# Kernel optimization log

Hardware: AMD Instinct MI355X
Metric: run time of the kernel (lower is better)

Reference implementation:

```python
import jax, jax.numpy as jnp
import numpy as np

SCALE = 2
K_UP = 5
PAD_UNF = (K_UP // 2) * SCALE  # nn.Unfold padding = k_up//2 * scale = 4
BN_INV = float(1.0 / np.sqrt(1.0 + 1e-5))  # BN inference with running_mean=0, running_var=1


def conv2d(x, w, pad):
    return jax.lax.conv_general_dilated(
        x, w, window_strides=(1, 1), padding=[(pad, pad), (pad, pad)],
        dimension_numbers=('NCHW', 'OIHW', 'NCHW'))


def bn(x, g, b):
    return x * (g * BN_INV)[None, :, None, None] + b[None, :, None, None]


def upsample_bilinear_ac(x, oh, ow):
    # bilinear, align_corners=True
    b, c, h, w = x.shape
    ys = jnp.linspace(0.0, h - 1.0, oh)
    xs = jnp.linspace(0.0, w - 1.0, ow)
    y0 = jnp.floor(ys).astype(jnp.int32)
    x0 = jnp.floor(xs).astype(jnp.int32)
    y1 = jnp.minimum(y0 + 1, h - 1)
    x1 = jnp.minimum(x0 + 1, w - 1)
    wy = (ys - y0)[:, None]  # (oh,1)
    wx = (xs - x0)          # (ow,)
    top = x[:, :, y0, :]
    bot = x[:, :, y1, :]
    top = top[:, :, :, x0] * (1.0 - wx) + top[:, :, :, x1] * wx
    bot = bot[:, :, :, x0] * (1.0 - wx) + bot[:, :, :, x1] * wx
    return top * (1.0 - wy) + bot * wy


def setup_inputs() -> dict:
    key = jax.random.key(0)
    ks = jax.random.split(key, 16)
    B, N, C = 4, 4096, 128  # h=w=64
    CL, CM, OUT = 128, 64, 128
    R = C // 4

    def rn(k, shape, s=0.05):
        return s * jax.random.normal(k, shape, dtype=jnp.float32)

    d = {}
    d['x_h'] = rn(ks[0], (B, N, C), 1.0)
    d['x_l'] = rn(ks[1], (B, N * SCALE * SCALE, CL), 1.0)
    # conv_reduce 3x3 C->C
    d['wr'] = rn(ks[2], (C, C, 3, 3))
    d['wr_g'] = jnp.ones((C,), jnp.float32); d['wr_b'] = jnp.zeros((C,), jnp.float32)
    # conv1 1x1 C->CM
    d['w1'] = rn(ks[3], (CM, C, 1, 1))
    d['w1_g'] = jnp.ones((CM,), jnp.float32); d['w1_b'] = jnp.zeros((CM,), jnp.float32)
    # conv2 1x1 2*CL->CM
    d['w2'] = rn(ks[4], (CM, 2 * CL, 1, 1))
    d['w2_g'] = jnp.ones((CM,), jnp.float32); d['w2_b'] = jnp.zeros((CM,), jnp.float32)
    # enc 3x3 2*CM -> k_up^2
    d['we'] = rn(ks[5], (K_UP * K_UP, 2 * CM, 3, 3))
    d['we_g'] = jnp.ones((K_UP * K_UP,), jnp.float32); d['we_b'] = jnp.zeros((K_UP * K_UP,), jnp.float32)
    # channel attention fc1/fc2 (1x1 convs with bias)
    d['wf1'] = rn(ks[6], (R, C, 1, 1)); d['bf1'] = jnp.zeros((R,), jnp.float32)
    d['wf2'] = rn(ks[7], (C, R, 1, 1)); d['bf2'] = jnp.zeros((C,), jnp.float32)
    # conv_out: 3x3 (C+CL)->OUT, then 1x1 OUT->OUT
    d['wo1'] = rn(ks[8], (OUT, C + CL, 3, 3))
    d['wo1_g'] = jnp.ones((OUT,), jnp.float32); d['wo1_b'] = jnp.zeros((OUT,), jnp.float32)
    d['wo2'] = rn(ks[9], (OUT, OUT, 1, 1))
    d['wo2_g'] = jnp.ones((OUT,), jnp.float32); d['wo2_b'] = jnp.zeros((OUT,), jnp.float32)
    return d


def reference(x_h, x_l, wr, wr_g, wr_b, w1, w1_g, w1_b, w2, w2_g, w2_b,
              we, we_g, we_b, wf1, bf1, wf2, bf2,
              wo1, wo1_g, wo1_b, wo2, wo2_g, wo2_b):
    B, N, C = x_h.shape
    h = int(round(N ** 0.5)); w = h
    h_, w_ = h * SCALE, w * SCALE
    xh = jnp.transpose(x_h, (0, 2, 1)).reshape(B, C, h, w)
    xl = jnp.transpose(x_l, (0, 2, 1)).reshape(B, -1, h_, w_)

    # x1 = upsample(conv1(x_h))
    x1 = upsample_bilinear_ac(jax.nn.relu(bn(conv2d(xh, w1, 0), w1_g, w1_b)), h_, w_)

    # channel attention on x_l
    g_c = jnp.mean(xl, axis=(2, 3), keepdims=True)  # (B,CL,1,1)
    g_c = conv2d(g_c, wf1, 0) + bf1[None, :, None, None]
    g_c = jax.nn.relu(g_c)
    g_c = conv2d(g_c, wf2, 0) + bf2[None, :, None, None]
    g_c = jax.nn.sigmoid(g_c) * xl

    x2 = jax.nn.relu(bn(conv2d(jnp.concatenate((g_c, xl), axis=1), w2, 0), w2_g, w2_b))

    # kernel prediction + softmax over k_up^2
    Wk = bn(conv2d(jnp.concatenate((x1, x2), axis=1), we, 1), we_g, we_b)
    Wk = jax.nn.softmax(Wk, axis=1)  # (B, 25, h_, w_)

    # reduce + upsample high-res feature
    xr = jax.nn.relu(bn(conv2d(xh, wr, 1), wr_g, wr_b))
    xup = upsample_bilinear_ac(xr, h_, w_)  # (B, C, h_, w_)

    # CARAFE-style reassembly: accumulate over k_up^2 dilated offsets
    xp = jnp.pad(xup, ((0, 0), (0, 0), (PAD_UNF, PAD_UNF), (PAD_UNF, PAD_UNF)))
    X = jnp.zeros_like(xup)
    idx = 0
    for i in range(K_UP):
        for j in range(K_UP):
            patch = xp[:, :, i * SCALE:i * SCALE + h_, j * SCALE:j * SCALE + w_]
            X = X + patch * Wk[:, idx][:, None]
            idx += 1

    y = jnp.concatenate((X, xl), axis=1)
    y = jax.nn.relu(bn(conv2d(y, wo1, 1), wo1_g, wo1_b))
    y = jax.nn.relu(bn(conv2d(y, wo2, 0), wo2_g, wo2_b))
    return y
```

## Files before the change

### kernel.cpp

```cpp
#include <hip/hip_runtime.h>
#include <hip/hip_bf16.h>

#define BN_INV 0.99999500003749968f

typedef __attribute__((ext_vector_type(8))) short bf16x8;
typedef __attribute__((ext_vector_type(4))) float f32x4;
typedef __attribute__((ext_vector_type(8))) unsigned short ushort8;
typedef unsigned short u16;

__device__ inline u16 f2bf(float f) {
  union { float f; unsigned int u; } v;
  v.f = f;
  unsigned int r = v.u + 0x7FFFu + ((v.u >> 16) & 1u);
  return (u16)(r >> 16);
}
__device__ inline float bf2f(u16 u) {
  union { unsigned int u; float f; } v;
  v.u = ((unsigned int)u) << 16;
  return v.f;
}
__device__ inline float asf(unsigned int u) {
  union { unsigned int u; float f; } v; v.u = u; return v.f;
}
__device__ inline void unpack8(bf16x8 v, float* f) {
  union { bf16x8 v; unsigned int w[4]; } u; u.v = v;
#pragma unroll
  for (int q = 0; q < 4; ++q) {
    f[2 * q]     = asf(u.w[q] << 16);
    f[2 * q + 1] = asf(u.w[q] & 0xFFFF0000u);
  }
}

#define GLOAD_LDS16(g, l)                                              \
  __builtin_amdgcn_global_load_lds(                                    \
      (const __attribute__((address_space(1))) unsigned int*)(g),      \
      (__attribute__((address_space(3))) unsigned int*)(l), 16, 0, 0)

__global__ __launch_bounds__(256) void k_zero_ring_all(
    u16* __restrict__ pad, u16* __restrict__ xcat, u16* __restrict__ xhp) {
  int blk = blockIdx.x;
  u16* buf; int PADW, CH, nb, b0;
  if (blk < 32)      { buf = pad;  PADW = 130; CH = 256; nb = 32; b0 = 0; }
  else if (blk < 48) { buf = xcat; PADW = 130; CH = 128; nb = 16; b0 = 32; }
  else               { buf = xhp;  PADW = 66;  CH = 128; nb = 8;  b0 = 48; }
  int nring = 2 * PADW + 2 * (PADW - 2);
  int vecs = CH >> 3;
  int total = 4 * nring * vecs;
  ushort8 z = {0, 0, 0, 0, 0, 0, 0, 0};
  for (int i = (blk - b0) * 256 + threadIdx.x; i < total; i += nb * 256) {
    int v = i % vecs;
    int r = (i / vecs) % nring;
    int b = i / (vecs * nring);
    int y, x;
    if (r < PADW) { y = 0; x = r; }
    else if (r < 2 * PADW) { y = PADW - 1; x = r - PADW; }
    else { int s = r - 2 * PADW; y = 1 + (s >> 1); x = (s & 1) ? (PADW - 1) : 0; }
    *(ushort8*)(buf + ((size_t)(b * PADW + y) * PADW + x) * CH + v * 8) = z;
  }
}

__global__ __launch_bounds__(256) void k_repack_all(
    const float* __restrict__ wr, const float* __restrict__ wrg,
    const float* __restrict__ we, const float* __restrict__ weg,
    const float* __restrict__ wo1, const float* __restrict__ wo1g,
    const float* __restrict__ wo2, const float* __restrict__ wo2g,
    const float* __restrict__ w1, const float* __restrict__ w1g,
    u16* __restrict__ wr_bf, u16* __restrict__ we_bf, u16* __restrict__ wo1bf,
    u16* __restrict__ wo2bf, u16* __restrict__ w1bf) {
  int blk = blockIdx.x;
  const float *w, *g; u16* out; int Cout, Cin, OPAD, TAPS, base;
  if (blk < 576)       { w = wr;  g = wrg;  out = wr_bf; Cout = 128; Cin = 128; OPAD = 128; TAPS = 9; base = 0; }
  else if (blk < 720)  { w = we;  g = weg;  out = we_bf; Cout = 25;  Cin = 128; OPAD = 32;  TAPS = 9; base = 576; }
  else if (blk < 1872) { w = wo1; g = wo1g; out = wo1bf; Cout = 128; Cin = 256; OPAD = 128; TAPS = 9; base = 720; }
  else if (blk < 1936) { w = wo2; g = wo2g; out = wo2bf; Cout = 128; Cin = 128; OPAD = 128; TAPS = 1; base = 1872; }
  else                 { w = w1;  g = w1g;  out = w1bf;  Cout = 64;  Cin = 128; OPAD = 64;  TAPS = 1; base = 1936; }
  int idx = (blk - base) * 256 + threadIdx.x;
  int c = idx % Cin;
  int o = (idx / Cin) % OPAD;
  int tap = idx / (Cin * OPAD);
  float v = 0.f;
  if (o < Cout) v = w[(o * Cin + c) * TAPS + tap] * g[o] * BN_INV;
  out[idx] = f2bf(v);
}

template <int PADW, int CIN, int NOUT, int NB, int TILE_M, int EPI, int NTHR,
          int WAVES_N>
__global__ __launch_bounds__(NTHR, 1) void k_conv_mfma(
    const u16* __restrict__ pad, const u16* __restrict__ wb,
    const float* __restrict__ bias, void* __restrict__ outp) {
  constexpr int H = PADW - 2;
  constexpr int NSEG = NOUT / NB;
  constexpr int KQ = CIN / 64;
  constexpr int NSTEPS = 9 * KQ;
  constexpr int NWAVES = NTHR / 64;
  constexpr int WAVES_M = NWAVES / WAVES_N;
  constexpr int WN = NB / WAVES_N;
  constexpr int NF = WN / 16;
  constexpr int WM = TILE_M / WAVES_M;
  constexpr int MF = WM / 16;
  constexpr int GRID = 4 * H * NSEG;
  constexpr int CPX = GRID / 8;
  constexpr int ALOADS = TILE_M * 8;
  constexpr int BLOADS = NB * 8;
  __shared__ alignas(16) u16 As[2][TILE_M * 64];
  __shared__ alignas(16) u16 Bs[2][NB * 64];

  int tid = threadIdx.x, wv = tid >> 6, l = tid & 63;
  int wrw = wv / WAVES_N, wc = wv % WAVES_N;
  int bid0 = blockIdx.x;
  int bid = (bid0 & 7) * CPX + (bid0 >> 3);
  int ns = (NSEG > 1) ? (bid % NSEG) : 0;
  int row = (NSEG > 1) ? (bid / NSEG) : bid;
  int b = row / H, y = row % H;
  const u16* pbat = pad + (size_t)b * PADW * PADW * CIN;

  auto stage = [&](int t, int bufi) {
    int tap = t / KQ;
    int ch0 = (t % KQ) * 64;
    int ky = tap / 3, kx = tap % 3;
    const u16* arow = pbat + ((size_t)(y + ky) * PADW + kx) * CIN + ch0;
#pragma unroll
    for (int j = 0; j < ALOADS / NTHR; ++j) {
      int q = j * NTHR + tid;
      int px = q >> 3;
      int sl = (q & 7) ^ (px & 7);
      GLOAD_LDS16(arow + (size_t)px * CIN + sl * 8,
                  (char*)&As[bufi][0] + (size_t)(j * NTHR + (tid & ~63)) * 16);
    }
    const u16* brow = wb + ((size_t)tap * NOUT + ns * NB) * CIN + ch0;
#pragma unroll
    for (int j = 0; j < BLOADS / NTHR; ++j) {
      int q = j * NTHR + tid;
      int co = q >> 3;
      int sl = (q & 7) ^ (co & 7);
      GLOAD_LDS16(brow + (size_t)co * CIN + sl * 8,
                  (char*)&Bs[bufi][0] + (size_t)(j * NTHR + (tid & ~63)) * 16);
    }
    if constexpr (BLOADS % NTHR) {
      if (tid < BLOADS % NTHR) {
        int q = (BLOADS / NTHR) * NTHR + tid;
        int co = q >> 3;
        int sl = (q & 7) ^ (co & 7);
        GLOAD_LDS16(brow + (size_t)co * CIN + sl * 8,
                    (char*)&Bs[bufi][0] +
                        (size_t)((BLOADS / NTHR) * NTHR + (tid & ~63)) * 16);
      }
    }
  };

  f32x4 acc[MF][NF];
#pragma unroll
  for (int m = 0; m < MF; ++m)
#pragma unroll
    for (int n = 0; n < NF; ++n) acc[m][n] = (f32x4){0.f, 0.f, 0.f, 0.f};

  stage(0, 0);
  for (int t = 0; t < NSTEPS; ++t) {
    __syncthreads();
    if (t + 1 < NSTEPS) stage(t + 1, (t + 1) & 1);
    const u16* Ab = &As[t & 1][0];
    const u16* Bb = &Bs[t & 1][0];
    bf16x8 Bf[2][NF];
#pragma unroll
    for (int kf = 0; kf < 2; ++kf)
#pragma unroll
      for (int n = 0; n < NF; ++n) {
        int co = wc * WN + n * 16 + (l & 15);
        int sl = (kf * 4 + (l >> 4)) ^ (co & 7);
        Bf[kf][n] = *(const bf16x8*)((const char*)Bb + co * 128 + sl * 16);
      }
#pragma unroll
    for (int m = 0; m < MF; ++m) {
      int px = wrw * WM + m * 16 + (l & 15);
      int s0 = (l >> 4) ^ (px & 7);
      int s1 = (4 + (l >> 4)) ^ (px & 7);
      bf16x8 a0 = *(const bf16x8*)((const char*)Ab + px * 128 + s0 * 16);
      bf16x8 a1 = *(const bf16x8*)((const char*)Ab + px * 128 + s1 * 16);
#pragma unroll
      for (int n = 0; n < NF; ++n) {
        acc[m][n] = __builtin_amdgcn_mfma_f32_16x16x32_bf16(a0, Bf[0][n], acc[m][n], 0, 0, 0);
        acc[m][n] = __builtin_amdgcn_mfma_f32_16x16x32_bf16(a1, Bf[1][n], acc[m][n], 0, 0, 0);
      }
    }
  }

  int ncol = l & 15, rq = l >> 4;
  size_t pixb = ((size_t)b * H + y) * H;
  if constexpr (EPI == 0) {
    u16* ob = (u16*)outp;
#pragma unroll
    for (int m = 0; m < MF; ++m) {
      int px0 = wrw * WM + m * 16 + rq * 4;
#pragma unroll
      for (int n = 0; n < NF; ++n) {
        int o = ns * NB + wc * WN + n * 16 + ncol;
        float be = bias[o];
#pragma unroll
        for (int r = 0; r < 4; ++r)
          ob[(pixb + px0 + r) * NOUT + o] = f2bf(fmaxf(acc[m][n][r] + be, 0.f));
      }
    }
  } else {
    float* sm = (float*)&As[0][0];
    __syncthreads();
#pragma unroll
    for (int m = 0; m < MF; ++m) {
      int px0 = wrw * WM + m * 16 + rq * 4;
#pragma unroll
      for (int n = 0; n < NF; ++n) {
        int o = wc * WN + n * 16 + ncol;
        float be = (o < 25) ? bias[o] : 0.f;
#pragma unroll
        for (int r = 0; r < 4; ++r)
          sm[(px0 + r) * 33 + o] = acc[m][n][r] + be;
      }
    }
    __syncthreads();
    if (tid < TILE_M) {
      int px = tid;
      float v[25];
      float mx = -1e30f;
#pragma unroll
      for (int i = 0; i < 25; ++i) {
        v[i] = sm[px * 33 + i];
        mx = fmaxf(mx, v[i]);
      }
      float s = 0.f;
#pragma unroll
      for (int i = 0; i < 25; ++i) {
        v[i] = expf(v[i] - mx);
        s += v[i];
      }
      float inv = 1.f / s;
      float* wkp = (float*)outp + (pixb + px) * 25;
#pragma unroll
      for (int i = 0; i < 25; ++i) wkp[i] = v[i] * inv;
    }
  }
}

__global__ __launch_bounds__(256) void k_stage_in(
    const float* __restrict__ xh, const float* __restrict__ xl,
    u16* __restrict__ xhp, u16* __restrict__ pad, float* __restrict__ gpart) {
  int blk = blockIdx.x;
  int tid = threadIdx.x;
  if (blk < 1024) {
    int idx = blk * 256 + tid;
    int c0 = (idx & 15) * 8;
    int p = idx >> 4;
    int b = p >> 12, pp = p & 4095;
    int y = pp >> 6, x = pp & 63;
    const float* s = xh + (size_t)p * 128 + c0;
    ushort8 o;
#pragma unroll
    for (int j = 0; j < 8; ++j) o[j] = f2bf(s[j]);
    *(ushort8*)(xhp + ((size_t)(b * 66 + y + 1) * 66 + (x + 1)) * 128 + c0) = o;
    return;
  }
  int blk2 = blk - 1024;
  int c0 = (tid & 15) * 8;
  int pxl = tid >> 4;
  int b = (blk2 * 64) >> 14;
  float facc[8] = {0.f, 0.f, 0.f, 0.f, 0.f, 0.f, 0.f, 0.f};
#pragma unroll
  for (int it = 0; it < 4; ++it) {
    int p = blk2 * 64 + it * 16 + pxl;
    int pp = p & 16383;
    int y = pp >> 7, x = pp & 127;
    const float* s = xl + (size_t)p * 128 + c0;
    ushort8 o;
#pragma unroll
    for (int j = 0; j < 8; ++j) {
      float f = s[j];
      facc[j] += f;
      o[j] = f2bf(f);
    }
    *(ushort8*)(pad + ((size_t)(b * 130 + y + 1) * 130 + (x + 1)) * 256 + 128 + c0) = o;
  }
  __shared__ float red[16][16][9];
#pragma unroll
  for (int j = 0; j < 8; ++j) red[pxl][tid & 15][j] = facc[j];
  __syncthreads();
  if (tid < 128) {
    float sum = 0.f;
#pragma unroll
    for (int q = 0; q < 16; ++q) sum += red[q][tid >> 3][tid & 7];
    atomicAdd(&gpart[(size_t)(blk2 & 63) * 512 + b * 128 + tid], sum);
  }
}

__global__ __launch_bounds__(128) void k_semlp(
    const float* __restrict__ gpart, const float* __restrict__ wf1,
    const float* __restrict__ bf1, const float* __restrict__ wf2,
    const float* __restrict__ bf2, const float* __restrict__ w2,
    const float* __restrict__ w2g, u16* __restrict__ weffb) {
  int b = blockIdx.x;
  int t = threadIdx.x;
  __shared__ float m[128], hid[32], sg[128];
  float s0 = 0.f;
  for (int s = 0; s < 64; ++s) s0 += gpart[(size_t)s * 512 + b * 128 + t];
  m[t] = s0 * (1.0f / 16384.0f);
  __syncthreads();
  if (t < 32) {
    float a = 0.f;
    for (int c = 0; c < 128; ++c) a += wf1[t * 128 + c] * m[c];
    hid[t] = fmaxf(a + bf1[t], 0.f);
  }
  __syncthreads();
  {
    float a = 0.f;
    for (int r = 0; r < 32; ++r) a += wf2[t * 32 + r] * hid[r];
    a += bf2[t];
    sg[t] = 1.f / (1.f + expf(-a));
  }
  __syncthreads();
  for (int o = 0; o < 64; ++o) {
    float sc = w2g[o] * BN_INV;
    weffb[((size_t)b * 64 + o) * 128 + t] =
        f2bf((w2[o * 256 + t] * sg[t] + w2[o * 256 + 128 + t]) * sc);
  }
}

__global__ __launch_bounds__(256) void k_t1x2(
    const u16* __restrict__ xhp, const u16* __restrict__ w1b,
    const float* __restrict__ w1bias, float* __restrict__ t1,
    const u16* __restrict__ pad, const u16* __restrict__ weffb,
    const float* __restrict__ x2bias, u16* __restrict__ xcat_pad) {
  int t = threadIdx.x;
  int wv = t >> 6, l = t & 63;
  int kg = l >> 4;
  if (blockIdx.x < 256) {
    int blk = blockIdx.x;
    int b = blk >> 6, y = blk & 63;
    int m0 = wv * 16;
    int xc = m0 + (l & 15);
    const u16* abase = xhp + ((size_t)(b * 66 + y + 1) * 66 + xc + 1) * 128 + kg * 8;
    const u16* bbase = w1b + (size_t)(l & 15) * 128 + kg * 8;
    f32x4 acc[4];
#pragma unroll
    for (int i = 0; i < 4; ++i) acc[i] = (f32x4){0.f, 0.f, 0.f, 0.f};
#pragma unroll
    for (int cc = 0; cc < 4; ++cc) {
      bf16x8 a = *(const bf16x8*)(abase + cc * 32);
#pragma unroll
      for (int nf = 0; nf < 4; ++nf) {
        bf16x8 bfr = *(const bf16x8*)(bbase + nf * 16 * 128 + cc * 32);
        acc[nf] = __builtin_amdgcn_mfma_f32_16x16x32_bf16(a, bfr, acc[nf], 0, 0, 0);
      }
    }
    int prow = m0 + (l >> 4) * 4;
    int ncol = l & 15;
    size_t pixb = ((size_t)b << 12) + ((size_t)y << 6);
#pragma unroll
    for (int nf = 0; nf < 4; ++nf) {
      int o = nf * 16 + ncol;
      float be = w1bias[o];
#pragma unroll
      for (int r = 0; r < 4; ++r)
        t1[(pixb + prow + r) * 64 + o] = fmaxf(acc[nf][r] + be, 0.f);
    }
    return;
  }
  int blk = blockIdx.x - 256;
  int b = blk >> 8, rr = blk & 255;
  int y = rr >> 1;
  int xseg = (rr & 1) << 6;
  int m0 = xseg + wv * 16;
  int xc = m0 + (l & 15);
  const u16* abase =
      pad + ((size_t)(b * 130 + y + 1) * 130 + xc + 1) * 256 + 128 + kg * 8;
  const u16* bbase = weffb + (size_t)b * 64 * 128 + (size_t)(l & 15) * 128 + kg * 8;
  f32x4 acc[4];
#pragma unroll
  for (int i = 0; i < 4; ++i) acc[i] = (f32x4){0.f, 0.f, 0.f, 0.f};
#pragma unroll
  for (int cc = 0; cc < 4; ++cc) {
    bf16x8 a = *(const bf16x8*)(abase + cc * 32);
#pragma unroll
    for (int nf = 0; nf < 4; ++nf) {
      bf16x8 bfr = *(const bf16x8*)(bbase + nf * 16 * 128 + cc * 32);
      acc[nf] = __builtin_amdgcn_mfma_f32_16x16x32_bf16(a, bfr, acc[nf], 0, 0, 0);
    }
  }
  int prow = m0 + (l >> 4) * 4;
  int ncol = l & 15;
  size_t rb = (size_t)(b * 130 + y + 1) * 130;
#pragma unroll
  for (int nf = 0; nf < 4; ++nf) {
    int o = nf * 16 + ncol;
    float be = x2bias[o];
#pragma unroll
    for (int r = 0; r < 4; ++r)
      xcat_pad[(rb + prow + r + 1) * 128 + 64 + o] =
          f2bf(fmaxf(acc[nf][r] + be, 0.f));
  }
}

__global__ __launch_bounds__(256) void k_up64_pad(const float* __restrict__ in,
                                                  u16* __restrict__ pad) {
  int t = threadIdx.x;
  int cp = (t & 31) * 2;
  int sub = t >> 5;
  int g = blockIdx.x * 8 + sub;
  int b = g >> 14, pp = g & 16383;
  int oy = pp >> 7, ox = pp & 127;
  const float S = 63.0f / 127.0f;
  float fy = oy * S, fx = ox * S;
  int y0 = (int)fy, x0 = (int)fx;
  int y1 = min(y0 + 1, 63), x1 = min(x0 + 1, 63);
  float wy = fy - y0, wx = fx - x0;
  const float* base = in + (size_t)b * 4096 * 64;
  float2 v00 = *(const float2*)(base + ((y0 << 6) + x0) * 64 + cp);
  float2 v01 = *(const float2*)(base + ((y0 << 6) + x1) * 64 + cp);
  float2 v10 = *(const float2*)(base + ((y1 << 6) + x0) * 64 + cp);
  float2 v11 = *(const float2*)(base + ((y1 << 6) + x1) * 64 + cp);
  float r0 = (v00.x * (1.f - wx) + v01.x * wx) * (1.f - wy) +
             (v10.x * (1.f - wx) + v11.x * wx) * wy;
  float r1 = (v00.y * (1.f - wx) + v01.y * wx) * (1.f - wy) +
             (v10.y * (1.f - wx) + v11.y * wx) * wy;
  ushort2 o2; o2.x = f2bf(r0); o2.y = f2bf(r1);
  *(ushort2*)(pad + ((size_t)(b * 130 + oy + 1) * 130 + ox + 1) * 128 + cp) = o2;
}

__global__ __launch_bounds__(256) void k_up128_bf(
    const u16* __restrict__ in, u16* __restrict__ outb) {
  int t = threadIdx.x;
  int c0 = (t & 15) * 8;
  int px = t >> 4;
  int g = blockIdx.x * 16 + px;
  int b = g >> 14, pp = g & 16383;
  int oy = pp >> 7, ox = pp & 127;
  const float S = 63.0f / 127.0f;
  float fy = oy * S, fx = ox * S;
  int y0 = (int)fy, x0 = (int)fx;
  int y1 = min(y0 + 1, 63), x1 = min(x0 + 1, 63);
  float wy = fy - y0, wx = fx - x0;
  const u16* base = in + (size_t)b * 4096 * 128 + c0;
  bf16x8 v00 = *(const bf16x8*)(base + ((y0 << 6) + x0) * 128);
  bf16x8 v01 = *(const bf16x8*)(base + ((y0 << 6) + x1) * 128);
  bf16x8 v10 = *(const bf16x8*)(base + ((y1 << 6) + x0) * 128);
  bf16x8 v11 = *(const bf16x8*)(base + ((y1 << 6) + x1) * 128);
  float f00[8], f01[8], f10[8], f11[8];
  unpack8(v00, f00); unpack8(v01, f01); unpack8(v10, f10); unpack8(v11, f11);
  ushort8 o;
#pragma unroll
  for (int j = 0; j < 8; ++j) {
    float top = f00[j] * (1.f - wx) + f01[j] * wx;
    float bot = f10[j] * (1.f - wx) + f11[j] * wx;
    o[j] = f2bf(top * (1.f - wy) + bot * wy);
  }
  *(ushort8*)(outb + (size_t)g * 128 + c0) = o;
}

__global__ __launch_bounds__(256) void k_carafe_bf(
    const u16* __restrict__ xup, const float* __restrict__ wk,
    u16* __restrict__ pad) {
  int t = threadIdx.x;
  int c0 = (t & 15) * 8;
  int px = t >> 4;
  int blk = (blockIdx.x & 7) * 512 + (blockIdx.x >> 3);
  int g = blk * 16 + px;
  int b = g >> 14, pp = g & 16383;
  int y = pp >> 7, x = pp & 127;
  __shared__ float wl[16][26];
  for (int i = t; i < 400; i += 256)
    wl[i / 25][i % 25] = wk[(size_t)(blk * 16 + i / 25) * 25 + (i % 25)];
  __syncthreads();
  float acc[8] = {0.f, 0.f, 0.f, 0.f, 0.f, 0.f, 0.f, 0.f};
  const u16* base = xup + ((size_t)b << 14) * 128 + c0;
#pragma unroll
  for (int i = 0; i < 5; ++i) {
    int row = y + 2 * i - 4;
    if ((unsigned)row >= 128u) continue;
#pragma unroll
    for (int jj = 0; jj < 5; ++jj) {
      int col = x + 2 * jj - 4;
      if ((unsigned)col >= 128u) continue;
      bf16x8 v = *(const bf16x8*)(base + (size_t)((row << 7) + col) * 128);
      float w = wl[px][i * 5 + jj];
      float f[8];
      unpack8(v, f);
#pragma unroll
      for (int k = 0; k < 8; ++k) acc[k] += w * f[k];
    }
  }
  ushort8 o;
#pragma unroll
  for (int k = 0; k < 8; ++k) o[k] = f2bf(acc[k]);
  *(ushort8*)(pad + ((size_t)(b * 130 + y + 1) * 130 + (x + 1)) * 256 + c0) = o;
}

__global__ __launch_bounds__(256) void k_wo2_mfma(
    const u16* __restrict__ y1, const u16* __restrict__ wb,
    const float* __restrict__ bb, float* __restrict__ out) {
  int t = threadIdx.x;
  int wv = t >> 6, l = t & 63;
  int blk = blockIdx.x;
  int b = blk >> 8, rr = blk & 255;
  int y = rr >> 1;
  int xseg = (rr & 1) << 6;
  int m0 = xseg + wv * 16;
  int xc = m0 + (l & 15);
  int kg = l >> 4;
  const u16* abase =
      y1 + ((size_t)((b << 14) + (y << 7) + xc)) * 128 + kg * 8;
  const u16* bbase = wb + (size_t)(l & 15) * 128 + kg * 8;
  f32x4 acc[8];
#pragma unroll
  for (int i = 0; i < 8; ++i) acc[i] = (f32x4){0.f, 0.f, 0.f, 0.f};
#pragma unroll
  for (int cc = 0; cc < 4; ++cc) {
    bf16x8 a = *(const bf16x8*)(abase + cc * 32);
#pragma unroll
    for (int nf = 0; nf < 8; ++nf) {
      bf16x8 bfr = *(const bf16x8*)(bbase + nf * 16 * 128 + cc * 32);
      acc[nf] = __builtin_amdgcn_mfma_f32_16x16x32_bf16(a, bfr, acc[nf], 0, 0, 0);
    }
  }
  __shared__ float lds[128 * 65];
  int lpx0 = wv * 16 + (l >> 4) * 4;
  int ncol = l & 15;
#pragma unroll
  for (int nf = 0; nf < 8; ++nf) {
    int o = nf * 16 + ncol;
    float be = bb[o];
#pragma unroll
    for (int r = 0; r < 4; ++r)
      lds[o * 65 + lpx0 + r] = fmaxf(acc[nf][r] + be, 0.f);
  }
  __syncthreads();
  size_t obase = (((size_t)(b * 128)) * 128 + y) * 128 + xseg;
#pragma unroll
  for (int rep = 0; rep < 8; ++rep) {
    int idx = rep * 256 + t;
    int o = idx >> 4;
    int x4 = (idx & 15) * 4;
    f32x4 v;
#pragma unroll
    for (int k = 0; k < 4; ++k) v[k] = lds[o * 65 + x4 + k];
    *(f32x4*)(out + obase + (size_t)o * 16384 + x4) = v;
  }
}

extern "C" void kernel_launch(void* const* d_in, const int* in_sizes, int n_in,
                              void* d_out, int out_size, void* d_ws,
                              size_t ws_size, hipStream_t stream) {
  const float* x_h  = (const float*)d_in[0];
  const float* x_l  = (const float*)d_in[1];
  const float* wr   = (const float*)d_in[2];
  const float* wr_g = (const float*)d_in[3];
  const float* wr_b = (const float*)d_in[4];
  const float* w1   = (const float*)d_in[5];
  const float* w1_g = (const float*)d_in[6];
  const float* w1_b = (const float*)d_in[7];
  const float* w2   = (const float*)d_in[8];
  const float* w2_g = (const float*)d_in[9];
  const float* w2_b = (const float*)d_in[10];
  const float* we   = (const float*)d_in[11];
  const float* we_g = (const float*)d_in[12];
  const float* we_b = (const float*)d_in[13];
  const float* wf1  = (const float*)d_in[14];
  const float* bf1  = (const float*)d_in[15];
  const float* wf2  = (const float*)d_in[16];
  const float* bf2  = (const float*)d_in[17];
  const float* wo1  = (const float*)d_in[18];
  const float* wo1_g= (const float*)d_in[19];
  const float* wo1_b= (const float*)d_in[20];
  const float* wo2  = (const float*)d_in[21];
  const float* wo2_g= (const float*)d_in[22];
  const float* wo2_b= (const float*)d_in[23];
  float* out = (float*)d_out;

  float* ws = (float*)d_ws;
  u16* pad      = (u16*)ws;
  u16* xcat_pad = (u16*)(ws + 8652800);
  u16* xup      = xcat_pad;
  float* wkb   = ws + 12979200;
  float* t1    = ws + 14617600;
  u16* xr = (u16*)t1;
  float* y1reg = ws + 15666176;
  u16* y1     = (u16*)y1reg;
  u16* xh_pad = (u16*)y1reg;
  float* gpart = ws + 19860480;
  u16* weff_bf = (u16*)(gpart + 32768);
  float* tail  = gpart + 32768 + 16384;
  u16* wr_bf = (u16*)tail;
  u16* we_bf = (u16*)(tail + 73728);
  u16* wo1bf = (u16*)(tail + 73728 + 18432);
  u16* wo2bf = (u16*)(tail + 73728 + 18432 + 147456);
  u16* w1bf  = (u16*)(tail + 73728 + 18432 + 147456 + 8192);

  hipMemsetAsync(gpart, 0, 32768 * sizeof(float), stream);
  k_zero_ring_all<<<56, 256, 0, stream>>>(pad, xcat_pad, xh_pad);
  k_repack_all<<<1968, 256, 0, stream>>>(wr, wr_g, we, we_g, wo1, wo1_g,
                                         wo2, wo2_g, w1, w1_g,
                                         wr_bf, we_bf, wo1bf, wo2bf, w1bf);

  k_stage_in<<<2048, 256, 0, stream>>>(x_h, x_l, xh_pad, pad, gpart);
  k_semlp<<<4, 128, 0, stream>>>(gpart, wf1, bf1, wf2, bf2, w2, w2_g, weff_bf);
  k_t1x2<<<1280, 256, 0, stream>>>(xh_pad, w1bf, w1_b, t1,
                                   pad, weff_bf, w2_b, xcat_pad);
  k_up64_pad<<<8192, 256, 0, stream>>>(t1, xcat_pad);

  k_conv_mfma<130, 128, 32, 32, 128, 2, 512, 2><<<512, 512, 0, stream>>>(
      xcat_pad, we_bf, we_b, wkb);
  k_conv_mfma<66, 128, 128, 64, 64, 0, 512, 4><<<512, 512, 0, stream>>>(
      xh_pad, wr_bf, wr_b, xr);
  k_up128_bf<<<4096, 256, 0, stream>>>(xr, xup);
  k_carafe_bf<<<4096, 256, 0, stream>>>(xup, wkb, pad);
  k_conv_mfma<130, 256, 128, 128, 128, 0, 512, 4><<<512, 512, 0, stream>>>(
      pad, wo1bf, wo1_b, y1);
  k_wo2_mfma<<<1024, 256, 0, stream>>>(y1, wo2bf, wo2_b, out);
}
```

Measured before the change: 190.2 us.

## Add dedicated wo1 conv kernel with row-halo LDS staging and prepacked MFMA weight fragments

Replaces the generic MFMA conv for the 256-to-128 channel 3x3 output conv with a specialized kernel. Each block computes one output row, stages three padded input rows per 64-channel chunk into swizzled LDS, and reuses them across all 9 taps. Weights are prepacked into per-lane MFMA fragment order so B operands load straight from global memory without LDS. This is meant to cut redundant input staging and weight shuffling, at the cost of keeping weight loads in global/L2 traffic and having no double buffering between chunks.

```diff
diff --git a/kernel.cpp b/kernel.cpp
--- a/kernel.cpp
+++ b/kernel.cpp
@@ -62,18 +62,16 @@
 __global__ __launch_bounds__(256) void k_repack_all(
     const float* __restrict__ wr, const float* __restrict__ wrg,
     const float* __restrict__ we, const float* __restrict__ weg,
-    const float* __restrict__ wo1, const float* __restrict__ wo1g,
     const float* __restrict__ wo2, const float* __restrict__ wo2g,
     const float* __restrict__ w1, const float* __restrict__ w1g,
-    u16* __restrict__ wr_bf, u16* __restrict__ we_bf, u16* __restrict__ wo1bf,
+    u16* __restrict__ wr_bf, u16* __restrict__ we_bf,
     u16* __restrict__ wo2bf, u16* __restrict__ w1bf) {
   int blk = blockIdx.x;
   const float *w, *g; u16* out; int Cout, Cin, OPAD, TAPS, base;
-  if (blk < 576)       { w = wr;  g = wrg;  out = wr_bf; Cout = 128; Cin = 128; OPAD = 128; TAPS = 9; base = 0; }
-  else if (blk < 720)  { w = we;  g = weg;  out = we_bf; Cout = 25;  Cin = 128; OPAD = 32;  TAPS = 9; base = 576; }
-  else if (blk < 1872) { w = wo1; g = wo1g; out = wo1bf; Cout = 128; Cin = 256; OPAD = 128; TAPS = 9; base = 720; }
-  else if (blk < 1936) { w = wo2; g = wo2g; out = wo2bf; Cout = 128; Cin = 128; OPAD = 128; TAPS = 1; base = 1872; }
-  else                 { w = w1;  g = w1g;  out = w1bf;  Cout = 64;  Cin = 128; OPAD = 64;  TAPS = 1; base = 1936; }
+  if (blk < 576)      { w = wr;  g = wrg;  out = wr_bf; Cout = 128; Cin = 128; OPAD = 128; TAPS = 9; base = 0; }
+  else if (blk < 720) { w = we;  g = weg;  out = we_bf; Cout = 25;  Cin = 128; OPAD = 32;  TAPS = 9; base = 576; }
+  else if (blk < 784) { w = wo2; g = wo2g; out = wo2bf; Cout = 128; Cin = 128; OPAD = 128; TAPS = 1; base = 720; }
+  else                { w = w1;  g = w1g;  out = w1bf;  Cout = 64;  Cin = 128; OPAD = 64;  TAPS = 1; base = 784; }
   int idx = (blk - base) * 256 + threadIdx.x;
   int c = idx % Cin;
   int o = (idx / Cin) % OPAD;
@@ -81,6 +79,21 @@
   float v = 0.f;
   if (o < Cout) v = w[(o * Cin + c) * TAPS + tap] * g[o] * BN_INV;
   out[idx] = f2bf(v);
+}
+
+__global__ __launch_bounds__(256) void k_repack_wo1frag(
+    const float* __restrict__ w, const float* __restrict__ g,
+    u16* __restrict__ out) {
+  int idx = blockIdx.x * 256 + threadIdx.x;
+  int e   = idx & 7;
+  int l   = (idx >> 3) & 63;
+  int kf  = (idx >> 9) & 1;
+  int nf  = (idx >> 10) & 7;
+  int cq  = (idx >> 13) & 3;
+  int tap = idx >> 15;
+  int o = nf * 16 + (l & 15);
+  int c = cq * 64 + (kf * 4 + (l >> 4)) * 8 + e;
+  out[idx] = f2bf(w[(o * 256 + c) * 9 + tap] * g[o] * BN_INV);
 }
 
 template <int PADW, int CIN, int NOUT, int NB, int TILE_M, int EPI, int NTHR,
@@ -235,6 +248,94 @@
       float* wkp = (float*)outp + (pixb + px) * 25;
 #pragma unroll
       for (int i = 0; i < 25; ++i) wkp[i] = v[i] * inv;
+    }
+  }
+}
+
+__global__ __launch_bounds__(512, 1) void k_wo1_conv(
+    const u16* __restrict__ pad, const u16* __restrict__ bfrag,
+    const float* __restrict__ bias, u16* __restrict__ y1) {
+  __shared__ alignas(16) u16 As[3 * 1056 * 8];
+  int tid = threadIdx.x, wv = tid >> 6, l = tid & 63;
+  int wrw = wv >> 2, wc = wv & 3;
+  int bid0 = blockIdx.x;
+  int bid = (bid0 & 7) * 64 + (bid0 >> 3);
+  int b = bid >> 7, y = bid & 127;
+  const u16* pbat = pad + (size_t)b * 130 * 130 * 256;
+
+  f32x4 acc[4][2];
+#pragma unroll
+  for (int m = 0; m < 4; ++m)
+#pragma unroll
+    for (int n = 0; n < 2; ++n) acc[m][n] = (f32x4){0.f, 0.f, 0.f, 0.f};
+
+  for (int cq = 0; cq < 4; ++cq) {
+    __syncthreads();
+    {
+      const u16* base = pbat + (size_t)y * 130 * 256 + cq * 64;
+#pragma unroll
+      for (int j = 0; j < 6; ++j) {
+        int q = j * 512 + tid;
+        int r = q / 1056;
+        int s = q - r * 1056;
+        int px = s >> 3;
+        int sl = (s & 7) ^ (px & 7);
+        GLOAD_LDS16(base + ((size_t)r * 130 + px) * 256 + sl * 8,
+                    (char*)As + (size_t)(j * 512 + (tid & ~63)) * 16);
+      }
+      if (tid < 96) {
+        int q = 3072 + tid;
+        int r = q / 1056;
+        int s = q - r * 1056;
+        int px = s >> 3;
+        int sl = (s & 7) ^ (px & 7);
+        GLOAD_LDS16(base + ((size_t)r * 130 + px) * 256 + sl * 8,
+                    (char*)As + (size_t)(3072 + (tid & ~63)) * 16);
+      }
+    }
+    __syncthreads();
+
+#pragma unroll
+    for (int tap = 0; tap < 9; ++tap) {
+      int ky = tap / 3, kx = tap % 3;
+      bf16x8 Bf[2][2];
+#pragma unroll
+      for (int kf = 0; kf < 2; ++kf)
+#pragma unroll
+        for (int n = 0; n < 2; ++n) {
+          int nf = wc * 2 + n;
+          Bf[kf][n] = *(const bf16x8*)(bfrag +
+              (((((size_t)tap * 4 + cq) * 8 + nf) * 2 + kf) * 64 + l) * 8);
+        }
+      const u16* arow = As + (size_t)ky * 1056 * 8;
+#pragma unroll
+      for (int m = 0; m < 4; ++m) {
+        int px = wrw * 64 + m * 16 + (l & 15) + kx;
+        int s0 = (l >> 4) ^ (px & 7);
+        int s1 = (4 + (l >> 4)) ^ (px & 7);
+        bf16x8 a0 = *(const bf16x8*)(arow + ((size_t)px * 8 + s0) * 8);
+        bf16x8 a1 = *(const bf16x8*)(arow + ((size_t)px * 8 + s1) * 8);
+#pragma unroll
+        for (int n = 0; n < 2; ++n) {
+          acc[m][n] = __builtin_amdgcn_mfma_f32_16x16x32_bf16(a0, Bf[0][n], acc[m][n], 0, 0, 0);
+          acc[m][n] = __builtin_amdgcn_mfma_f32_16x16x32_bf16(a1, Bf[1][n], acc[m][n], 0, 0, 0);
+        }
+      }
+    }
+  }
+
+  int ncol = l & 15, rq2 = l >> 4;
+  size_t pixb = ((size_t)b * 128 + y) * 128;
+#pragma unroll
+  for (int m = 0; m < 4; ++m) {
+    int px0 = wrw * 64 + m * 16 + rq2 * 4;
+#pragma unroll
+    for (int n = 0; n < 2; ++n) {
+      int o = wc * 32 + n * 16 + ncol;
+      float be = bias[o];
+#pragma unroll
+      for (int r = 0; r < 4; ++r)
+        y1[(pixb + px0 + r) * 128 + o] = f2bf(fmaxf(acc[m][n][r] + be, 0.f));
     }
   }
 }
@@ -592,9 +693,10 @@
 
   hipMemsetAsync(gpart, 0, 32768 * sizeof(float), stream);
   k_zero_ring_all<<<56, 256, 0, stream>>>(pad, xcat_pad, xh_pad);
-  k_repack_all<<<1968, 256, 0, stream>>>(wr, wr_g, we, we_g, wo1, wo1_g,
-                                         wo2, wo2_g, w1, w1_g,
-                                         wr_bf, we_bf, wo1bf, wo2bf, w1bf);
+  k_repack_all<<<816, 256, 0, stream>>>(wr, wr_g, we, we_g,
+                                        wo2, wo2_g, w1, w1_g,
+                                        wr_bf, we_bf, wo2bf, w1bf);
+  k_repack_wo1frag<<<1152, 256, 0, stream>>>(wo1, wo1_g, wo1bf);
 
   k_stage_in<<<2048, 256, 0, stream>>>(x_h, x_l, xh_pad, pad, gpart);
   k_semlp<<<4, 128, 0, stream>>>(gpart, wf1, bf1, wf2, bf2, w2, w2_g, weff_bf);
@@ -608,7 +710,6 @@
       xh_pad, wr_bf, wr_b, xr);
   k_up128_bf<<<4096, 256, 0, stream>>>(xr, xup);
   k_carafe_bf<<<4096, 256, 0, stream>>>(xup, wkb, pad);
-  k_conv_mfma<130, 256, 128, 128, 128, 0, 512, 4><<<512, 512, 0, stream>>>(
-      pad, wo1bf, wo1_b, y1);
+  k_wo1_conv<<<512, 512, 0, stream>>>(pad, wo1bf, wo1_b, y1);
   k_wo2_mfma<<<1024, 256, 0, stream>>>(y1, wo2bf, wo2_b, out);
 }
```

Measured after the change: 197.1 us. +3.6%, slower.
